# Kernel tuning notes

Hardware: AMD Instinct MI355X
Metric: run time of the kernel (lower is better)

The kernel has to match this reference:

```python
import jax, jax.numpy as jnp
import numpy as np

N_NODES = 50000
N_EDGES = 600000
N_FEAT = 128
NHID = 128
N_CLASSES = 10
N_GRAPHS = 512
BN_EPS = 1e-5


def _gcn_conv(x, W, b, src, dst, n):
    """PyG GCNConv: D^{-1/2}(A+I)D^{-1/2} X W + b (symmetric norm, self-loops)."""
    xw = x @ W  # [n, out]
    deg = jax.ops.segment_sum(jnp.ones(src.shape[0], x.dtype), dst, num_segments=n) + 1.0
    dinv = jax.lax.rsqrt(deg)  # [n]
    norm = dinv[src] * dinv[dst]  # [E]
    agg = jax.ops.segment_sum(xw[src] * norm[:, None], dst, num_segments=n)
    agg = agg + xw * (dinv * dinv)[:, None]  # self-loop contribution
    return agg + b


def setup_inputs() -> dict:
    key = jax.random.key(0)
    ks = jax.random.split(key, 16)
    s_in = 1.0 / np.sqrt(N_FEAT)
    s_h = 1.0 / np.sqrt(NHID)
    s_h2 = 1.0 / np.sqrt(NHID // 2)
    return {
        "x": jax.random.normal(ks[0], (N_NODES, N_FEAT), jnp.float32),
        "edge_index": jax.random.randint(ks[1], (2, N_EDGES), 0, N_NODES, jnp.int32),
        "batch": jnp.sort(jax.random.randint(ks[2], (N_NODES,), 0, N_GRAPHS, jnp.int32)),
        "W1": jax.random.normal(ks[3], (N_FEAT, NHID), jnp.float32) * s_in,
        "b1": jnp.zeros((NHID,), jnp.float32),
        "W2": jax.random.normal(ks[4], (NHID, NHID), jnp.float32) * s_h,
        "b2": jnp.zeros((NHID,), jnp.float32),
        "W3": jax.random.normal(ks[5], (NHID, NHID), jnp.float32) * s_h,
        "b3": jnp.zeros((NHID,), jnp.float32),
        "gamma": jnp.ones((NHID,), jnp.float32),
        "beta": jnp.zeros((NHID,), jnp.float32),
        "run_mean": jnp.zeros((NHID,), jnp.float32),
        "run_var": jnp.ones((NHID,), jnp.float32),
        "lw1": jax.random.normal(ks[6], (NHID, NHID), jnp.float32) * s_h,
        "lb1": jnp.zeros((NHID,), jnp.float32),
        "lw2": jax.random.normal(ks[7], (NHID, NHID // 2), jnp.float32) * s_h,
        "lb2": jnp.zeros((NHID // 2,), jnp.float32),
        "lw3": jax.random.normal(ks[8], (NHID // 2, N_CLASSES), jnp.float32) * s_h2,
        "lb3": jnp.zeros((N_CLASSES,), jnp.float32),
    }


def reference(x, edge_index, batch, W1, b1, W2, b2, W3, b3,
              gamma, beta, run_mean, run_var,
              lw1, lb1, lw2, lb2, lw3, lb3):
    src, dst = edge_index[0], edge_index[1]
    h = jax.nn.relu(_gcn_conv(x, W1, b1, src, dst, N_NODES))
    h = jax.nn.relu(_gcn_conv(h, W2, b2, src, dst, N_NODES))
    h = jax.nn.relu(_gcn_conv(h, W3, b3, src, dst, N_NODES))
    # BatchNorm1d (eval: running stats)
    h = (h - run_mean) * jax.lax.rsqrt(run_var + BN_EPS) * gamma + beta
    # scatter_max over graph ids -> [N_GRAPHS, NHID]
    g = jax.ops.segment_max(h, batch, num_segments=N_GRAPHS)
    g = jax.nn.relu(g @ lw1 + lb1)
    g = jax.nn.relu(g @ lw2 + lb2)
    return g @ lw3 + lb3
```

## Files before the change

kernel.cpp:

```cpp
#include <hip/hip_runtime.h>
#include <hip/hip_bf16.h>

#define NHID 128
#define NGRAPH 512
#define NCLS 10

typedef __attribute__((ext_vector_type(8))) short bf16x8;
typedef __attribute__((ext_vector_type(4))) float f32x4;
typedef __attribute__((ext_vector_type(4))) unsigned int u32x4;

__device__ inline unsigned int fenc(float f) {
    unsigned int u = __float_as_uint(f);
    return (u & 0x80000000u) ? ~u : (u | 0x80000000u);
}
__device__ inline float fdec(unsigned int u) {
    u = (u & 0x80000000u) ? (u & 0x7fffffffu) : ~u;
    return __uint_as_float(u);
}
__device__ inline unsigned short f2bf(float f) {
    unsigned int u = __float_as_uint(f);
    return (unsigned short)((u + 0x7fffu + ((u >> 16) & 1u)) >> 16);
}
__device__ inline unsigned int packbf(float lo, float hi) {
    return (unsigned)f2bf(lo) | ((unsigned)f2bf(hi) << 16);
}

__global__ void k_deg(const int* __restrict__ dst, int* __restrict__ cnt, int E) {
    int e = blockIdx.x * blockDim.x + threadIdx.x;
    if (e < E) atomicAdd(&cnt[dst[e]], 1);
}

__global__ __launch_bounds__(1024) void k_scan1(const int* __restrict__ cnt,
        float* __restrict__ dinv, int* __restrict__ rowptr,
        int* __restrict__ bsum, int N) {
    __shared__ int lds[1024];
    int t = threadIdx.x;
    int i = blockIdx.x * 1024 + t;
    int v = (i < N) ? cnt[i] : 0;
    if (i < N) dinv[i] = rsqrtf((float)v + 1.0f);
    lds[t] = v;
    __syncthreads();
    for (int off = 1; off < 1024; off <<= 1) {
        int x = (t >= off) ? lds[t - off] : 0;
        __syncthreads();
        lds[t] += x;
        __syncthreads();
    }
    if (i < N) rowptr[i + 1] = lds[t];
    if (t == 1023) bsum[blockIdx.x] = lds[1023];
}

__global__ __launch_bounds__(1024) void k_scan2(int* __restrict__ bsum, int nb) {
    __shared__ int lds[1024];
    int t = threadIdx.x;
    int v = (t < nb) ? bsum[t] : 0;
    lds[t] = v;
    __syncthreads();
    for (int off = 1; off < 1024; off <<= 1) {
        int x = (t >= off) ? lds[t - off] : 0;
        __syncthreads();
        lds[t] += x;
        __syncthreads();
    }
    if (t < nb) bsum[t] = lds[t] - v;
}

__global__ void k_scan3(int* __restrict__ rowptr, const int* __restrict__ bsum, int N) {
    int i = blockIdx.x * 256 + threadIdx.x;
    if (i < N) rowptr[i + 1] += bsum[i >> 10];
    if (i == 0) rowptr[0] = 0;
}

__global__ void k_fill(const int* __restrict__ src, const int* __restrict__ dst,
                       const float* __restrict__ dinv, const int* __restrict__ rowptr,
                       int* __restrict__ cursor, int2* __restrict__ csr, int E) {
    int e = blockIdx.x * blockDim.x + threadIdx.x;
    if (e >= E) return;
    int s = src[e], d = dst[e];
    int pos = rowptr[d] + atomicAdd(&cursor[d], 1);
    csr[pos] = make_int2(s, __float_as_int(dinv[s] * dinv[d]));
}

__global__ void k_prep(const float* __restrict__ x, unsigned int* __restrict__ xb, int n8,
                       const float* __restrict__ W1, const float* __restrict__ W2,
                       const float* __restrict__ W3, unsigned short* __restrict__ Wt) {
    int i = blockIdx.x * 256 + threadIdx.x;
    if (i < n8) {
        const float* p = x + (size_t)i * 8;
        f32x4 a = *reinterpret_cast<const f32x4*>(p);
        f32x4 b = *reinterpret_cast<const f32x4*>(p + 4);
        u32x4 o;
        o[0] = packbf(a[0], a[1]);
        o[1] = packbf(a[2], a[3]);
        o[2] = packbf(b[0], b[1]);
        o[3] = packbf(b[2], b[3]);
        *reinterpret_cast<u32x4*>(xb + (size_t)i * 4) = o;
    } else {
        int idx = i - n8;
        if (idx < 3 * 16384) {
            int l = idx >> 14;
            int r = idx & 16383;
            const float* W = (l == 0) ? W1 : (l == 1) ? W2 : W3;
            int c = r & 127, k = r >> 7;
            Wt[l * 16384 + c * NHID + k] = f2bf(W[k * NHID + c]);
        }
    }
}

__device__ inline void fma8(const u32x4& u, float nw, float* a) {
#pragma unroll
    for (int q = 0; q < 4; ++q) {
        a[2 * q]     = fmaf(nw, __uint_as_float(u[q] << 16), a[2 * q]);
        a[2 * q + 1] = fmaf(nw, __uint_as_float(u[q] & 0xffff0000u), a[2 * q + 1]);
    }
}

__global__ __launch_bounds__(256) void k_agg(const unsigned int* __restrict__ Hb,
        const int2* __restrict__ csr, const int* __restrict__ rowptr,
        const float* __restrict__ dinv, unsigned int* __restrict__ aggb, int N) {
    int w = (blockIdx.x * 256 + threadIdx.x) >> 6;
    if (w >= N) return;
    int lane = threadIdx.x & 63;
    int g = lane >> 4;
    int l16 = lane & 15;
    float a[8];
#pragma unroll
    for (int e = 0; e < 8; ++e) a[e] = 0.f;
    int beg = rowptr[w], end = rowptr[w + 1];
    int trips = (end - beg + 3) >> 2;
    int j = beg + g;
#pragma unroll 2
    for (int t = 0; t < trips; ++t, j += 4) {
        int s = w;
        float nw = 0.f;
        if (j < end) { int2 e2 = csr[j]; s = e2.x; nw = __int_as_float(e2.y); }
        u32x4 u = reinterpret_cast<const u32x4*>(Hb + (size_t)s * (NHID / 2))[l16];
        fma8(u, nw, a);
    }
    if (g == 0) {
        float di = dinv[w];
        u32x4 u = reinterpret_cast<const u32x4*>(Hb + (size_t)w * (NHID / 2))[l16];
        fma8(u, di * di, a);
    }
#pragma unroll
    for (int e = 0; e < 8; ++e) {
        a[e] += __shfl_xor(a[e], 16);
        a[e] += __shfl_xor(a[e], 32);
    }
    if (g == 0) {
        u32x4 o;
        o[0] = packbf(a[0], a[1]);
        o[1] = packbf(a[2], a[3]);
        o[2] = packbf(a[4], a[5]);
        o[3] = packbf(a[6], a[7]);
        *reinterpret_cast<u32x4*>(aggb + (size_t)w * (NHID / 2) + l16 * 4) = o;
    }
}

__global__ __launch_bounds__(256) void k_gemm(const unsigned short* __restrict__ A,
        const unsigned short* __restrict__ Wt, const float* __restrict__ bias,
        unsigned short* __restrict__ Hb, int M) {
    int wave = threadIdx.x >> 6;
    int lane = threadIdx.x & 63;
    int lr = lane & 15;
    int kq = lane >> 4;
    int r0 = blockIdx.x * 64 + wave * 16;
    f32x4 acc[8];
#pragma unroll
    for (int nt = 0; nt < 8; ++nt) acc[nt] = 0.f;
    int ar = r0 + lr;
    bool arok = ar < M;
#pragma unroll
    for (int kg = 0; kg < 4; ++kg) {
        int kb = kg * 32 + kq * 8;
        bf16x8 af = bf16x8(0);
        if (arok) af = *reinterpret_cast<const bf16x8*>(A + (size_t)ar * NHID + kb);
#pragma unroll
        for (int nt = 0; nt < 8; ++nt) {
            bf16x8 bf = *reinterpret_cast<const bf16x8*>(Wt + (size_t)(nt * 16 + lr) * NHID + kb);
            acc[nt] = __builtin_amdgcn_mfma_f32_16x16x32_bf16(af, bf, acc[nt], 0, 0, 0);
        }
    }
#pragma unroll
    for (int nt = 0; nt < 8; ++nt) {
        int c = nt * 16 + lr;
        float b = bias[c];
#pragma unroll
        for (int e = 0; e < 4; ++e) {
            int r = r0 + kq * 4 + e;
            if (r < M) {
                float v = fmaxf(acc[nt][e] + b, 0.f);
                Hb[(size_t)r * NHID + c] = f2bf(v);
            }
        }
    }
}

__global__ __launch_bounds__(256) void k_bnmax(const unsigned short* __restrict__ Hb,
        const int* __restrict__ batch, const float* __restrict__ gamma,
        const float* __restrict__ beta, const float* __restrict__ rmean,
        const float* __restrict__ rvar, unsigned int* __restrict__ keys, int N) {
    int c = threadIdx.x & 127;
    int h = threadIdx.x >> 7;
    int n0 = blockIdx.x * 64;
    float sc = gamma[c] * rsqrtf(rvar[c] + 1e-5f);
    float sh = beta[c] - rmean[c] * sc;
    int cur = -1;
    float m = -3.0e38f;
    int nend = n0 + 64 < N ? n0 + 64 : N;
    for (int n = n0 + h; n < nend; n += 2) {
        int g = batch[n];
        if (g != cur) {
            if (cur >= 0) atomicMax(&keys[(size_t)cur * NHID + c], fenc(m));
            cur = g;
            m = -3.0e38f;
        }
        float hv = __uint_as_float(((unsigned)Hb[(size_t)n * NHID + c]) << 16);
        float y = fmaf(hv, sc, sh);
        m = fmaxf(m, y);
    }
    if (cur >= 0) atomicMax(&keys[(size_t)cur * NHID + c], fenc(m));
}

__global__ __launch_bounds__(128) void k_head(const unsigned int* __restrict__ keys,
        const float* __restrict__ lw1, const float* __restrict__ lb1,
        const float* __restrict__ lw2, const float* __restrict__ lb2,
        const float* __restrict__ lw3, const float* __restrict__ lb3,
        float* __restrict__ out) {
    __shared__ float g0[NHID], g1[NHID], g2[64];
    int r = blockIdx.x;
    int t = threadIdx.x;
    unsigned int u = keys[(size_t)r * NHID + t];
    g0[t] = (u == 0u) ? -3.0e38f : fdec(u);
    __syncthreads();
    float acc = lb1[t];
#pragma unroll 8
    for (int k = 0; k < NHID; ++k) acc = fmaf(g0[k], lw1[k * NHID + t], acc);
    g1[t] = fmaxf(acc, 0.f);
    __syncthreads();
    if (t < 64) {
        acc = lb2[t];
#pragma unroll 8
        for (int k = 0; k < NHID; ++k) acc = fmaf(g1[k], lw2[k * 64 + t], acc);
        g2[t] = fmaxf(acc, 0.f);
    }
    __syncthreads();
    if (t < NCLS) {
        acc = lb3[t];
#pragma unroll 8
        for (int k = 0; k < 64; ++k) acc = fmaf(g2[k], lw3[k * NCLS + t], acc);
        out[(size_t)r * NCLS + t] = acc;
    }
}

extern "C" void kernel_launch(void* const* d_in, const int* in_sizes, int n_in,
                              void* d_out, int out_size, void* d_ws, size_t ws_size,
                              hipStream_t stream) {
    const float* x     = (const float*)d_in[0];
    const int*   ei    = (const int*)d_in[1];
    const int*   batch = (const int*)d_in[2];
    const float* W1 = (const float*)d_in[3];
    const float* b1 = (const float*)d_in[4];
    const float* W2 = (const float*)d_in[5];
    const float* b2 = (const float*)d_in[6];
    const float* W3 = (const float*)d_in[7];
    const float* b3 = (const float*)d_in[8];
    const float* gamma = (const float*)d_in[9];
    const float* beta  = (const float*)d_in[10];
    const float* rmean = (const float*)d_in[11];
    const float* rvar  = (const float*)d_in[12];
    const float* lw1 = (const float*)d_in[13];
    const float* lb1 = (const float*)d_in[14];
    const float* lw2 = (const float*)d_in[15];
    const float* lb2 = (const float*)d_in[16];
    const float* lw3 = (const float*)d_in[17];
    const float* lb3 = (const float*)d_in[18];

    const int N = in_sizes[2];
    const int E = in_sizes[1] / 2;
    const int* src = ei;
    const int* dst = ei + E;

    char* ws = (char*)d_ws;
    size_t off = 0;
    auto alloc = [&](size_t bytes) {
        char* p = ws + off;
        off += (bytes + 255) & ~(size_t)255;
        return p;
    };
    int*   cnt     = (int*)  alloc((size_t)N * 8);
    int*   cursor  = cnt + N;
    int*   rowptr  = (int*)  alloc(((size_t)N + 1) * 4);
    int*   bsum    = (int*)  alloc(1024 * 4);
    float* dinv    = (float*)alloc((size_t)N * 4);
    int2*  csr     = (int2*) alloc((size_t)E * 8);
    unsigned int* xb   = (unsigned int*)alloc((size_t)N * NHID * 2);
    unsigned int* aggb = (unsigned int*)alloc((size_t)N * NHID * 2);
    unsigned int* Hb   = (unsigned int*)alloc((size_t)N * NHID * 2);
    unsigned short* Wt = (unsigned short*)alloc((size_t)3 * NHID * NHID * 2);
    unsigned int* keys = (unsigned int*)alloc((size_t)NGRAPH * NHID * 4);
    (void)ws_size; (void)n_in; (void)out_size;

    hipMemsetAsync(cnt, 0, (size_t)N * 8, stream);
    hipMemsetAsync(keys, 0, (size_t)NGRAPH * NHID * 4, stream);

    int eb = (E + 255) / 256;
    int nb1 = (N + 1023) / 1024;
    k_deg<<<eb, 256, 0, stream>>>(dst, cnt, E);
    k_scan1<<<nb1, 1024, 0, stream>>>(cnt, dinv, rowptr, bsum, N);
    k_scan2<<<1, 1024, 0, stream>>>(bsum, nb1);
    k_scan3<<<(N + 255) / 256, 256, 0, stream>>>(rowptr, bsum, N);
    k_fill<<<eb, 256, 0, stream>>>(src, dst, dinv, rowptr, cursor, csr, E);
    int n8 = N * 16;
    k_prep<<<(n8 + 3 * 16384 + 255) / 256, 256, 0, stream>>>(x, xb, n8, W1, W2, W3, Wt);

    int ab = ((size_t)N * 64 + 255) / 256;
    int gb = (N + 63) / 64;
    k_agg<<<ab, 256, 0, stream>>>(xb, csr, rowptr, dinv, aggb, N);
    k_gemm<<<gb, 256, 0, stream>>>((const unsigned short*)aggb, Wt, b1, (unsigned short*)Hb, N);
    k_agg<<<ab, 256, 0, stream>>>(Hb, csr, rowptr, dinv, aggb, N);
    k_gemm<<<gb, 256, 0, stream>>>((const unsigned short*)aggb, Wt + 16384, b2, (unsigned short*)Hb, N);
    k_agg<<<ab, 256, 0, stream>>>(Hb, csr, rowptr, dinv, aggb, N);
    k_gemm<<<gb, 256, 0, stream>>>((const unsigned short*)aggb, Wt + 32768, b3, (unsigned short*)Hb, N);

    k_bnmax<<<gb, 256, 0, stream>>>((const unsigned short*)Hb, batch, gamma, beta, rmean, rvar, keys, N);
    k_head<<<NGRAPH, 128, 0, stream>>>(keys, lw1, lb1, lw2, lb2, lw3, lb3, (float*)d_out);
}
```

Measured before the change: 280.5 us.

## Fuse final GEMM with batchnorm segment-max and batch four gathers in aggregation

The last GCN GEMM now applies bias, ReLU and the eval BatchNorm in registers, then reduces per-graph maxima in a shared-memory table before issuing global atomics. This removes the separate bnmax kernel and the round trip of the final hidden matrix through memory. The aggregation kernel now loads four neighbour rows per iteration per lane group, and prefetches the self-loop row, to raise memory-level parallelism. The 32KB shared table may reduce occupancy of the fused kernel, and it relies on sorted batch ids.

Result: faster. 249.3 us (-11.1%).

```diff
diff --git a/kernel.cpp b/kernel.cpp
--- a/kernel.cpp
+++ b/kernel.cpp
@@ -123,25 +123,31 @@
     int lane = threadIdx.x & 63;
     int g = lane >> 4;
     int l16 = lane & 15;
+    float di = dinv[w];
+    u32x4 us = reinterpret_cast<const u32x4*>(Hb + (size_t)w * (NHID / 2))[l16];
     float a[8];
 #pragma unroll
     for (int e = 0; e < 8; ++e) a[e] = 0.f;
     int beg = rowptr[w], end = rowptr[w + 1];
-    int trips = (end - beg + 3) >> 2;
+    int trips = (end - beg + 15) >> 4;
     int j = beg + g;
-#pragma unroll 2
-    for (int t = 0; t < trips; ++t, j += 4) {
-        int s = w;
-        float nw = 0.f;
-        if (j < end) { int2 e2 = csr[j]; s = e2.x; nw = __int_as_float(e2.y); }
-        u32x4 u = reinterpret_cast<const u32x4*>(Hb + (size_t)s * (NHID / 2))[l16];
-        fma8(u, nw, a);
-    }
-    if (g == 0) {
-        float di = dinv[w];
-        u32x4 u = reinterpret_cast<const u32x4*>(Hb + (size_t)w * (NHID / 2))[l16];
-        fma8(u, di * di, a);
-    }
+    for (int t = 0; t < trips; ++t, j += 16) {
+        int s0 = w, s1 = w, s2 = w, s3 = w;
+        float n0 = 0.f, n1 = 0.f, n2 = 0.f, n3 = 0.f;
+        if (j < end)      { int2 e2 = csr[j];      s0 = e2.x; n0 = __int_as_float(e2.y); }
+        if (j + 4 < end)  { int2 e2 = csr[j + 4];  s1 = e2.x; n1 = __int_as_float(e2.y); }
+        if (j + 8 < end)  { int2 e2 = csr[j + 8];  s2 = e2.x; n2 = __int_as_float(e2.y); }
+        if (j + 12 < end) { int2 e2 = csr[j + 12]; s3 = e2.x; n3 = __int_as_float(e2.y); }
+        u32x4 u0 = reinterpret_cast<const u32x4*>(Hb + (size_t)s0 * (NHID / 2))[l16];
+        u32x4 u1 = reinterpret_cast<const u32x4*>(Hb + (size_t)s1 * (NHID / 2))[l16];
+        u32x4 u2 = reinterpret_cast<const u32x4*>(Hb + (size_t)s2 * (NHID / 2))[l16];
+        u32x4 u3 = reinterpret_cast<const u32x4*>(Hb + (size_t)s3 * (NHID / 2))[l16];
+        fma8(u0, n0, a);
+        fma8(u1, n1, a);
+        fma8(u2, n2, a);
+        fma8(u3, n3, a);
+    }
+    if (g == 0) fma8(us, di * di, a);
 #pragma unroll
     for (int e = 0; e < 8; ++e) {
         a[e] += __shfl_xor(a[e], 16);
@@ -196,30 +202,67 @@
     }
 }
 
-__global__ __launch_bounds__(256) void k_bnmax(const unsigned short* __restrict__ Hb,
+__global__ __launch_bounds__(256) void k_gemm_bn(const unsigned short* __restrict__ A,
+        const unsigned short* __restrict__ Wt, const float* __restrict__ bias,
         const int* __restrict__ batch, const float* __restrict__ gamma,
         const float* __restrict__ beta, const float* __restrict__ rmean,
-        const float* __restrict__ rvar, unsigned int* __restrict__ keys, int N) {
-    int c = threadIdx.x & 127;
-    int h = threadIdx.x >> 7;
+        const float* __restrict__ rvar, unsigned int* __restrict__ keys, int M) {
+    __shared__ unsigned int smax[64][NHID];
+    __shared__ int bseg[64];
+    int tid = threadIdx.x;
     int n0 = blockIdx.x * 64;
-    float sc = gamma[c] * rsqrtf(rvar[c] + 1e-5f);
-    float sh = beta[c] - rmean[c] * sc;
-    int cur = -1;
-    float m = -3.0e38f;
-    int nend = n0 + 64 < N ? n0 + 64 : N;
-    for (int n = n0 + h; n < nend; n += 2) {
-        int g = batch[n];
-        if (g != cur) {
-            if (cur >= 0) atomicMax(&keys[(size_t)cur * NHID + c], fenc(m));
-            cur = g;
-            m = -3.0e38f;
-        }
-        float hv = __uint_as_float(((unsigned)Hb[(size_t)n * NHID + c]) << 16);
-        float y = fmaf(hv, sc, sh);
-        m = fmaxf(m, y);
-    }
-    if (cur >= 0) atomicMax(&keys[(size_t)cur * NHID + c], fenc(m));
+    for (int i = tid; i < 64 * NHID; i += 256) ((unsigned int*)smax)[i] = 0u;
+    if (tid < 64) {
+        int r = n0 + tid;
+        bseg[tid] = batch[r < M ? r : M - 1];
+    }
+    int wave = tid >> 6;
+    int lane = tid & 63;
+    int lr = lane & 15;
+    int kq = lane >> 4;
+    int r0 = n0 + wave * 16;
+    f32x4 acc[8];
+#pragma unroll
+    for (int nt = 0; nt < 8; ++nt) acc[nt] = 0.f;
+    int ar = r0 + lr;
+    bool arok = ar < M;
+#pragma unroll
+    for (int kg = 0; kg < 4; ++kg) {
+        int kb = kg * 32 + kq * 8;
+        bf16x8 af = bf16x8(0);
+        if (arok) af = *reinterpret_cast<const bf16x8*>(A + (size_t)ar * NHID + kb);
+#pragma unroll
+        for (int nt = 0; nt < 8; ++nt) {
+            bf16x8 bf = *reinterpret_cast<const bf16x8*>(Wt + (size_t)(nt * 16 + lr) * NHID + kb);
+            acc[nt] = __builtin_amdgcn_mfma_f32_16x16x32_bf16(af, bf, acc[nt], 0, 0, 0);
+        }
+    }
+    __syncthreads();
+    int glo = bseg[0];
+#pragma unroll
+    for (int nt = 0; nt < 8; ++nt) {
+        int c = nt * 16 + lr;
+        float b = bias[c];
+        float sc = gamma[c] * rsqrtf(rvar[c] + 1e-5f);
+        float sh = beta[c] - rmean[c] * sc;
+#pragma unroll
+        for (int e = 0; e < 4; ++e) {
+            int rr = wave * 16 + kq * 4 + e;
+            if (n0 + rr < M) {
+                float v = fmaxf(acc[nt][e] + b, 0.f);
+                float y = fmaf(v, sc, sh);
+                atomicMax(&smax[bseg[rr] - glo][c], fenc(y));
+            }
+        }
+    }
+    __syncthreads();
+    int last = M - 1 - n0;
+    if (last > 63) last = 63;
+    int span = bseg[last] - glo + 1;
+    for (int i = tid; i < span * NHID; i += 256) {
+        unsigned int v = ((unsigned int*)smax)[i];
+        if (v) atomicMax(&keys[(size_t)(glo + (i >> 7)) * NHID + (i & 127)], v);
+    }
 }
 
 __global__ __launch_bounds__(128) void k_head(const unsigned int* __restrict__ keys,
@@ -321,8 +364,8 @@
     k_agg<<<ab, 256, 0, stream>>>(Hb, csr, rowptr, dinv, aggb, N);
     k_gemm<<<gb, 256, 0, stream>>>((const unsigned short*)aggb, Wt + 16384, b2, (unsigned short*)Hb, N);
     k_agg<<<ab, 256, 0, stream>>>(Hb, csr, rowptr, dinv, aggb, N);
-    k_gemm<<<gb, 256, 0, stream>>>((const unsigned short*)aggb, Wt + 32768, b3, (unsigned short*)Hb, N);
-
-    k_bnmax<<<gb, 256, 0, stream>>>((const unsigned short*)Hb, batch, gamma, beta, rmean, rvar, keys, N);
+    k_gemm_bn<<<gb, 256, 0, stream>>>((const unsigned short*)aggb, Wt + 32768, b3,
+                                      batch, gamma, beta, rmean, rvar, keys, N);
+
     k_head<<<NGRAPH, 128, 0, stream>>>(keys, lw1, lb1, lw2, lb2, lw3, lb3, (float*)d_out);
 }
```
